# Optimization experiments

Hardware: AMD Instinct MI355X
Metric: run time of the kernel (lower is better)

## Reference

```python
import jax, jax.numpy as jnp
import numpy as np

# Config from init_kwargs
B = 16
CIN = 128
COUT = 256
N = 16        # num_filters
L = 32        # length
K = 3         # kernel_size
KAPPA = 4
STRIDE = 1
PAD = 2
LP = L + PAD  # padded spatial length for FFT


def make_wn():
    # DFT-derived channel-mixing matrix, (cin, d) with d = cout // n
    v = np.arange(CIN)[:, None]
    sr = N * CIN // COUT
    inds = np.arange(CIN)[np.arange(CIN) % sr == 0]
    M = v @ v[inds].T  # (cin, d)
    wn = np.exp((2j * np.pi / CIN) * M) / CIN
    return jnp.asarray(wn.astype(np.complex64))


def setup_inputs() -> dict:
    key = jax.random.key(0)
    k1, k2 = jax.random.split(key)
    x = jax.random.normal(k1, (B, CIN, L, L), dtype=jnp.float32)
    rng = float(np.sqrt(KAPPA / (CIN * K * K)))
    weight = (jax.random.uniform(k2, (N, CIN // KAPPA, K, K), dtype=jnp.float32) - 0.5) * 2.0 * rng
    return {"x": x, "weight": weight}


def reference(x, weight):
    wn = make_wn()  # complex64 (CIN, COUT//N), constant buffer
    # 3D real FFT over (channel, h, w); weight zero-padded from cin//kappa -> cin channels
    x_hat = jnp.fft.rfftn(x, s=(CIN, LP, LP), axes=(-3, -2, -1))          # (B, CIN, LP, LP//2+1)
    w_hat = jnp.fft.rfftn(weight, s=(CIN, LP, LP), axes=(-3, -2, -1))     # (N, CIN, LP, LP//2+1)
    freq = jnp.einsum('bchw,nchw->bnchw', x_hat, w_hat)                   # broadcast, no reduction
    out = jnp.fft.irfftn(freq, s=(LP, LP), axes=(-2, -1))                 # real (B, N, CIN, LP, LP)
    # complex channel mix contracting c -> d; result complex, take real part
    out = jnp.einsum('cd,bnchw->bndhw', wn, out)                          # (B, N, D, LP, LP) complex
    out = out.real[:, :, :, PAD:, PAD:]                                   # (B, N, D, L, L)
    out = jnp.transpose(out, (0, 2, 1, 3, 4))                             # (B, D, N, L, L)
    out = out.reshape(out.shape[0], -1, out.shape[3], out.shape[4])       # (B, COUT, L, L)
    if STRIDE == 2:
        idx = jnp.arange(0, L, 2)
        out = out[:, :, idx, :][:, :, :, idx]
    return out
```

## Files before the change

kernel.cpp:

```cpp
#include <hip/hip_runtime.h>
#include <hip/hip_bf16.h>


typedef __attribute__((ext_vector_type(8))) short short8;
typedef __attribute__((ext_vector_type(4))) float floatx4;

#define NT 256
#define SROW 35
#define SOCT (6 * SROW)

__global__ __launch_bounds__(576, 1)
void prep_weights(const float* __restrict__ wgt, short* __restrict__ wfg) {
    const int tid  = threadIdx.x;
    const int t    = tid >> 6;
    const int lane = tid & 63;
    const int n    = lane & 15;
    const int q    = lane >> 4;
    const int k    = 8 - t;
    short8 v;
#pragma unroll
    for (int j = 0; j < 8; ++j) {
        const int c2 = q * 8 + j;
        __hip_bfloat16 h = __float2bfloat16(wgt[(n * 32 + c2) * 9 + k]);
        v[j] = __builtin_bit_cast(short, h);
    }
    *(short8*)&wfg[tid * 8] = v;
}

__global__ __launch_bounds__(NT, 6)
void fconv_mfma(const float* __restrict__ x,
                const short* __restrict__ wfg,
                float* __restrict__ out) {
    __shared__ __align__(16) short xs[4 * SOCT * 8];

    const int band = blockIdx.x;
    const int d    = blockIdx.y;
    const int b    = blockIdx.z;
    const int r0   = band * 4;
    const int tid  = threadIdx.x;
    const int dup  = ((d & 7) == 0);
    const int lane = tid & 63;

    const float* xb_base = x + ((size_t)b << 17);

    if (tid < 192) {
        const int oct = tid / 48;
        const int rem = tid - oct * 48;
        const int sq  = rem / 6;
        const int r   = rem - sq * 6;
        const int gr  = r0 + r;
        union { __hip_bfloat162 h2[4]; short8 s8; } u[4];
        if (gr < 32) {
            const float* base = xb_base + (gr << 5) + (sq << 2);
#pragma unroll
            for (int half = 0; half < 2; ++half) {
                float va[4][4];
#pragma unroll
                for (int jj = 0; jj < 4; ++jj) {
                    const int c2  = oct * 8 + half * 4 + jj;
                    const int c1a = (8 * d - c2) & 127;
                    float4 A = *(const float4*)(base + (c1a << 10));
                    if (!dup) {
                        const int c1b = (-8 * d - c2) & 127;
                        const float4 Bv = *(const float4*)(base + (c1b << 10));
                        A.x = 0.5f * (A.x + Bv.x); A.y = 0.5f * (A.y + Bv.y);
                        A.z = 0.5f * (A.z + Bv.z); A.w = 0.5f * (A.w + Bv.w);
                    }
                    va[jj][0] = A.x; va[jj][1] = A.y;
                    va[jj][2] = A.z; va[jj][3] = A.w;
                }
#pragma unroll
                for (int ss = 0; ss < 4; ++ss)
#pragma unroll
                    for (int p = 0; p < 2; ++p)
                        u[ss].h2[half * 2 + p] = __float22bfloat162_rn(
                            make_float2(va[2 * p][ss], va[2 * p + 1][ss]));
            }
        } else {
#pragma unroll
            for (int ss = 0; ss < 4; ++ss)
#pragma unroll
                for (int j = 0; j < 8; ++j) u[ss].s8[j] = 0;
        }
#pragma unroll
        for (int ss = 0; ss < 4; ++ss)
            *(short8*)&xs[(oct * SOCT + r * SROW + (sq << 2) + ss) << 3] = u[ss].s8;
    }
    if (tid < 48) {
        const int oct = tid / 12;
        const int rem = tid - oct * 12;
        const int r   = rem >> 1;
        const int s   = 32 + (rem & 1);
        short8 z = {0, 0, 0, 0, 0, 0, 0, 0};
        *(short8*)&xs[(oct * SOCT + r * SROW + s) << 3] = z;
    }

    short8 af[9];
    const short8* wf8 = (const short8*)wfg;
#pragma unroll
    for (int t = 0; t < 9; ++t)
        af[t] = wf8[t * 64 + lane];

    __syncthreads();

    const int c = lane & 15;
    const int q = lane >> 4;
    const int w = tid >> 6;
#pragma unroll
    for (int i = 0; i < 2; ++i) {
        const int s0 = i << 4;
        floatx4 acc = {0.f, 0.f, 0.f, 0.f};
        const short* basep = &xs[(q * SOCT + w * SROW + s0 + c) << 3];
#pragma unroll
        for (int u = 0; u < 3; ++u)
#pragma unroll
            for (int v = 0; v < 3; ++v) {
                const short8 bf = *(const short8*)(basep + ((u * SROW + v) << 3));
                acc = __builtin_amdgcn_mfma_f32_16x16x32_bf16(af[u * 3 + v], bf, acc, 0, 0, 0);
            }
        float* op = out + (size_t)(((b * 256 + d * 16 + q * 4) * 32 + (r0 + w)) * 32 + s0 + c);
        op[0]    = acc.x;
        op[1024] = acc.y;
        op[2048] = acc.z;
        op[3072] = acc.w;
        if (d >= 1 && d <= 7) {
            float* op2 = op + (size_t)(16 - 2 * d) * 16384;
            op2[0]    = acc.x;
            op2[1024] = acc.y;
            op2[2048] = acc.z;
            op2[3072] = acc.w;
        }
    }
}

extern "C" void kernel_launch(void* const* d_in, const int* in_sizes, int n_in,
                              void* d_out, int out_size, void* d_ws, size_t ws_size,
                              hipStream_t stream) {
    const float* x   = (const float*)d_in[0];
    const float* wgt = (const float*)d_in[1];
    float* out = (float*)d_out;
    short* wfg = (short*)d_ws;
    (void)in_sizes; (void)n_in; (void)out_size; (void)ws_size;

    prep_weights<<<dim3(1), dim3(576), 0, stream>>>(wgt, wfg);

    dim3 grid(8, 9, 16);
    fconv_mfma<<<grid, dim3(NT), 0, stream>>>(x, wfg, out);
}
```

Before: 75.65 us.

## Fuse weight prep into conv kernel and reuse staged rows across all d

Removes the separate weight-prep launch; each block now converts the weights to bf16 fragments in registers. Each block stages two output rows of all 128 channels once in shared memory, laid out in a channel-wrapped order. It then loops over all nine d values, forming the two symmetric channel-shifted MFMA products instead of averaging the two shifted inputs beforehand. This avoids re-reading x from global memory for every d and drops one launch, at the cost of twice the MFMA work, a larger LDS footprint, lower occupancy and a smaller grid of 256 blocks.

Result: no change. 74.54 us (-1.5%).

```diff
diff --git a/kernel.cpp b/kernel.cpp
--- a/kernel.cpp
+++ b/kernel.cpp
@@ -6,119 +6,113 @@
 typedef __attribute__((ext_vector_type(4))) float floatx4;
 
 #define NT 256
-#define SROW 35
-#define SOCT (6 * SROW)
+#define LCH 168
+#define SROWS 34
+#define XSROW (SROWS * LCH)
 
-__global__ __launch_bounds__(576, 1)
-void prep_weights(const float* __restrict__ wgt, short* __restrict__ wfg) {
-    const int tid  = threadIdx.x;
-    const int t    = tid >> 6;
+__global__ __launch_bounds__(NT, 2)
+void fconv_mfma(const float* __restrict__ x,
+                const float* __restrict__ wgt,
+                float* __restrict__ out) {
+    __shared__ __align__(16) short xs[4 * XSROW];
+
+    const int rq  = blockIdx.x;
+    const int b   = blockIdx.y;
+    const int r0  = rq * 2;
+    const int tid = threadIdx.x;
     const int lane = tid & 63;
-    const int n    = lane & 15;
-    const int q    = lane >> 4;
-    const int k    = 8 - t;
-    short8 v;
+    const int wv  = tid >> 6;
+
+    const int n = lane & 15;
+    const int q = lane >> 4;
+
+    float wreg[72];
+    {
+        const float4* wp = (const float4*)(wgt + (n * 288 + q * 72));
 #pragma unroll
-    for (int j = 0; j < 8; ++j) {
-        const int c2 = q * 8 + j;
-        __hip_bfloat16 h = __float2bfloat16(wgt[(n * 32 + c2) * 9 + k]);
-        v[j] = __builtin_bit_cast(short, h);
+        for (int i = 0; i < 18; ++i) {
+            const float4 t4 = wp[i];
+            wreg[4 * i]     = t4.x; wreg[4 * i + 1] = t4.y;
+            wreg[4 * i + 2] = t4.z; wreg[4 * i + 3] = t4.w;
+        }
     }
-    *(short8*)&wfg[tid * 8] = v;
-}
+    short8 af[9];
+#pragma unroll
+    for (int t = 0; t < 9; ++t)
+#pragma unroll
+        for (int j = 0; j < 8; ++j) {
+            const int f = (7 - j) * 9 + (8 - t);
+            __hip_bfloat16 hh = __float2bfloat16(0.5f * wreg[f]);
+            af[t][j] = __builtin_bit_cast(short, hh);
+        }
 
-__global__ __launch_bounds__(NT, 6)
-void fconv_mfma(const float* __restrict__ x,
-                const short* __restrict__ wfg,
-                float* __restrict__ out) {
-    __shared__ __align__(16) short xs[4 * SOCT * 8];
-
-    const int band = blockIdx.x;
-    const int d    = blockIdx.y;
-    const int b    = blockIdx.z;
-    const int r0   = band * 4;
-    const int tid  = threadIdx.x;
-    const int dup  = ((d & 7) == 0);
-    const int lane = tid & 63;
-
-    const float* xb_base = x + ((size_t)b << 17);
-
-    if (tid < 192) {
-        const int oct = tid / 48;
-        const int rem = tid - oct * 48;
-        const int sq  = rem / 6;
-        const int r   = rem - sq * 6;
-        const int gr  = r0 + r;
-        union { __hip_bfloat162 h2[4]; short8 s8; } u[4];
-        if (gr < 32) {
-            const float* base = xb_base + (gr << 5) + (sq << 2);
+    const int ch = tid & 127;
+    const int h  = tid >> 7;
+    const bool w1 = (ch <= 64);
+    const bool w2 = (ch >= 33);
 #pragma unroll
-            for (int half = 0; half < 2; ++half) {
-                float va[4][4];
+    for (int rr = 0; rr < 2; ++rr) {
+        const int lrow = 2 * h + rr;
+        const int grow = r0 + lrow;
+        short* rowbase = &xs[lrow * XSROW];
+        if (grow < 32) {
+            const float* rowp = x + ((size_t)((b * 128 + ch) * 32 + grow) << 5);
 #pragma unroll
-                for (int jj = 0; jj < 4; ++jj) {
-                    const int c2  = oct * 8 + half * 4 + jj;
-                    const int c1a = (8 * d - c2) & 127;
-                    float4 A = *(const float4*)(base + (c1a << 10));
-                    if (!dup) {
-                        const int c1b = (-8 * d - c2) & 127;
-                        const float4 Bv = *(const float4*)(base + (c1b << 10));
-                        A.x = 0.5f * (A.x + Bv.x); A.y = 0.5f * (A.y + Bv.y);
-                        A.z = 0.5f * (A.z + Bv.z); A.w = 0.5f * (A.w + Bv.w);
-                    }
-                    va[jj][0] = A.x; va[jj][1] = A.y;
-                    va[jj][2] = A.z; va[jj][3] = A.w;
+            for (int cq = 0; cq < 8; ++cq) {
+                const float4 v4 = *(const float4*)(rowp + cq * 4);
+                const float vv[4] = {v4.x, v4.y, v4.z, v4.w};
+#pragma unroll
+                for (int e = 0; e < 4; ++e) {
+                    const int col = cq * 4 + e;
+                    __hip_bfloat16 hb = __float2bfloat16(vv[e]);
+                    const short hv = __builtin_bit_cast(short, hb);
+                    if (w1) rowbase[col * LCH + ch + 95] = hv;
+                    if (w2) rowbase[col * LCH + ch - 33] = hv;
                 }
-#pragma unroll
-                for (int ss = 0; ss < 4; ++ss)
-#pragma unroll
-                    for (int p = 0; p < 2; ++p)
-                        u[ss].h2[half * 2 + p] = __float22bfloat162_rn(
-                            make_float2(va[2 * p][ss], va[2 * p + 1][ss]));
             }
         } else {
 #pragma unroll
-            for (int ss = 0; ss < 4; ++ss)
-#pragma unroll
-                for (int j = 0; j < 8; ++j) u[ss].s8[j] = 0;
+            for (int col = 0; col < 32; ++col) {
+                if (w1) rowbase[col * LCH + ch + 95] = 0;
+                if (w2) rowbase[col * LCH + ch - 33] = 0;
+            }
         }
-#pragma unroll
-        for (int ss = 0; ss < 4; ++ss)
-            *(short8*)&xs[(oct * SOCT + r * SROW + (sq << 2) + ss) << 3] = u[ss].s8;
     }
-    if (tid < 48) {
-        const int oct = tid / 12;
-        const int rem = tid - oct * 12;
-        const int r   = rem >> 1;
-        const int s   = 32 + (rem & 1);
+    if (tid < 168) {
+        const int row = tid / 42;
+        const int g   = tid - row * 42;
         short8 z = {0, 0, 0, 0, 0, 0, 0, 0};
-        *(short8*)&xs[(oct * SOCT + r * SROW + s) << 3] = z;
+        *(short8*)&xs[(row * SROWS + 32) * LCH + g * 8] = z;
     }
-
-    short8 af[9];
-    const short8* wf8 = (const short8*)wfg;
-#pragma unroll
-    for (int t = 0; t < 9; ++t)
-        af[t] = wf8[t * 64 + lane];
 
     __syncthreads();
 
-    const int c = lane & 15;
-    const int q = lane >> 4;
-    const int w = tid >> 6;
-#pragma unroll
-    for (int i = 0; i < 2; ++i) {
-        const int s0 = i << 4;
-        floatx4 acc = {0.f, 0.f, 0.f, 0.f};
-        const short* basep = &xs[(q * SOCT + w * SROW + s0 + c) << 3];
+    const int lr = wv >> 1;
+    const int sh = wv & 1;
+    const int s0 = sh << 4;
+    const int bpi = (lr * SROWS + s0 + n) * LCH - 8 * q;
+
+    for (int d = 0; d <= 8; ++d) {
+        floatx4 a0 = {0.f, 0.f, 0.f, 0.f}, a1 = {0.f, 0.f, 0.f, 0.f};
+        floatx4 b0 = {0.f, 0.f, 0.f, 0.f}, b1 = {0.f, 0.f, 0.f, 0.f};
 #pragma unroll
         for (int u = 0; u < 3; ++u)
 #pragma unroll
             for (int v = 0; v < 3; ++v) {
-                const short8 bf = *(const short8*)(basep + ((u * SROW + v) << 3));
-                acc = __builtin_amdgcn_mfma_f32_16x16x32_bf16(af[u * 3 + v], bf, acc, 0, 0, 0);
+                const int t = u * 3 + v;
+                const int si = bpi + (u * SROWS + v) * LCH;
+                const short8 ba = *(const short8*)&xs[si + 8 * (11 + d)];
+                const short8 bb = *(const short8*)&xs[si + 8 * (11 - d)];
+                if (t & 1) {
+                    a1 = __builtin_amdgcn_mfma_f32_16x16x32_bf16(af[t], ba, a1, 0, 0, 0);
+                    b1 = __builtin_amdgcn_mfma_f32_16x16x32_bf16(af[t], bb, b1, 0, 0, 0);
+                } else {
+                    a0 = __builtin_amdgcn_mfma_f32_16x16x32_bf16(af[t], ba, a0, 0, 0, 0);
+                    b0 = __builtin_amdgcn_mfma_f32_16x16x32_bf16(af[t], bb, b0, 0, 0, 0);
+                }
             }
-        float* op = out + (size_t)(((b * 256 + d * 16 + q * 4) * 32 + (r0 + w)) * 32 + s0 + c);
+        const floatx4 acc = (a0 + a1) + (b0 + b1);
+        float* op = out + ((size_t)((b * 256 + d * 16 + q * 4) * 32 + (r0 + lr)) << 5) + s0 + n;
         op[0]    = acc.x;
         op[1024] = acc.y;
         op[2048] = acc.z;
@@ -139,11 +133,7 @@
     const float* x   = (const float*)d_in[0];
     const float* wgt = (const float*)d_in[1];
     float* out = (float*)d_out;
-    short* wfg = (short*)d_ws;
-    (void)in_sizes; (void)n_in; (void)out_size; (void)ws_size;
+    (void)in_sizes; (void)n_in; (void)out_size; (void)d_ws; (void)ws_size;
 
-    prep_weights<<<dim3(1), dim3(576), 0, stream>>>(wgt, wfg);
-
-    dim3 grid(8, 9, 16);
-    fconv_mfma<<<grid, dim3(NT), 0, stream>>>(x, wfg, out);
+    fconv_mfma<<<dim3(16, 16), dim3(NT), 0, stream>>>(x, wgt, out);
 }
```
